# Kernel optimization log

Measured on AMD Instinct MI355X. Metric: run time of the kernel, lower is better.

## Reference

```python
import jax, jax.numpy as jnp
import numpy as np

NU, EU = 40000, 640000          # user-graph nodes / edges
B, T, NW, ET = 64, 16, 30, 60    # users, tweets/user, words/tweet, edges/tweet
NT = B * T * NW                  # 30720 tweet word-nodes
NTE = B * T * ET                 # 61440 tweet edges
NSEG_T = B * T                   # 1024 tweet segments


def gcn_conv(x, src, dst, W, b, N):
    """PyG GCNConv: x@W, add self loops, sym deg-normalize, scatter-add, +b."""
    x = x @ W
    loop = jnp.arange(N)
    s = jnp.concatenate([src, loop])
    d = jnp.concatenate([dst, loop])
    deg = jax.ops.segment_sum(jnp.ones_like(d, dtype=x.dtype), d, num_segments=N)
    dinv = jnp.where(deg > 0, jax.lax.rsqrt(deg), 0.0)
    norm = dinv[s] * dinv[d]                     # [E+N]
    out = jax.ops.segment_sum(x[s] * norm[:, None], d, num_segments=N)
    return out + b


def att_pool(x, seg, nseg, W1, b1, W2, b2):
    """AttentionalAggregation: gate_nn = Linear->Linear, segment softmax, weighted sum."""
    gate = (x @ W1 + b1) @ W2 + b2               # [N, C]
    m = jax.ops.segment_max(gate, seg, num_segments=nseg)
    e = jnp.exp(gate - m[seg])
    s = jax.ops.segment_sum(e, seg, num_segments=nseg)
    a = e / (s[seg] + 1e-16)
    return jax.ops.segment_sum(a * x, seg, num_segments=nseg)  # [nseg, C]


def gru_last(x_seq, W_ih, W_hh, b_ih, b_hh):
    """torch.nn.GRU, 1 layer; x_seq [B,T,C] -> final hidden [B,C]."""
    C = W_hh.shape[1]
    h0 = jnp.zeros((x_seq.shape[0], C), x_seq.dtype)
    def step(h, x):
        gi = x @ W_ih.T + b_ih
        gh = h @ W_hh.T + b_hh
        ir, iz, inn = jnp.split(gi, 3, axis=-1)
        hr, hz, hn = jnp.split(gh, 3, axis=-1)
        r = jax.nn.sigmoid(ir + hr)
        z = jax.nn.sigmoid(iz + hz)
        n = jnp.tanh(inn + r * hn)
        return (1.0 - z) * n + z * h, None
    hT, _ = jax.lax.scan(step, h0, jnp.swapaxes(x_seq, 0, 1))
    return hT


def setup_inputs():
    ks = jax.random.split(jax.random.key(0), 24)
    def rn(i, shape, s=1.0):
        return jax.random.normal(ks[i], shape, dtype=jnp.float32) * s
    z = lambda n_: jnp.zeros((n_,), jnp.float32)
    inp = {}
    inp["user_x"] = rn(0, (NU, 128))
    inp["user_feats"] = rn(1, (B, 32))
    inp["tweet_x"] = rn(2, (NT, 768))
    inp["Wu0"] = rn(3, (128, 128), 0.1); inp["bu0"] = z(128)
    inp["Wu1"] = rn(4, (128, 128), 0.1); inp["bu1"] = z(128)
    inp["Wgu1"] = rn(5, (128, 128), 0.1); inp["bgu1"] = z(128)
    inp["Wgu2"] = rn(6, (128, 128), 0.1); inp["bgu2"] = z(128)
    inp["Wt0"] = rn(7, (768, 256), 0.05); inp["bt0"] = z(256)
    inp["Wt1"] = rn(8, (256, 128), 0.1); inp["bt1"] = z(128)
    inp["Wgt1"] = rn(9, (128, 128), 0.1); inp["bgt1"] = z(128)
    inp["Wgt2"] = rn(10, (128, 128), 0.1); inp["bgt2"] = z(128)
    inp["W_ih"] = rn(11, (384, 128), 0.1); inp["b_ih"] = z(384)
    inp["W_hh"] = rn(12, (384, 128), 0.1); inp["b_hh"] = z(384)
    inp["Wd0"] = rn(13, (288, 256), 0.1); inp["bd0"] = z(256)
    inp["Wd1"] = rn(14, (256, 64), 0.1); inp["bd1"] = z(64)
    inp["Wp"] = rn(15, (64, 1), 0.1); inp["bp"] = z(1)
    inp["user_edge_index"] = jax.random.randint(ks[16], (2, EU), 0, NU)
    local = jax.random.randint(ks[17], (2, NTE), 0, NW)
    offs = jnp.repeat(jnp.arange(NSEG_T) * NW, ET)   # edges stay inside each tweet
    inp["tweet_edge_index"] = local + offs[None, :]
    inp["user_batch"] = jnp.arange(NU) // (NU // B)  # contiguous per-user segments (ptr)
    inp["tweet_batch"] = jnp.arange(NT) // NW        # contiguous per-tweet segments (ptr)
    return inp


def reference(user_x, user_feats, tweet_x,
              Wu0, bu0, Wu1, bu1, Wgu1, bgu1, Wgu2, bgu2,
              Wt0, bt0, Wt1, bt1, Wgt1, bgt1, Wgt2, bgt2,
              W_ih, b_ih, W_hh, b_hh,
              Wd0, bd0, Wd1, bd1, Wp, bp,
              user_edge_index, tweet_edge_index, user_batch, tweet_batch):
    h = jax.nn.relu(gcn_conv(user_x, user_edge_index[0], user_edge_index[1], Wu0, bu0, NU))
    h = jax.nn.relu(gcn_conv(h, user_edge_index[0], user_edge_index[1], Wu1, bu1, NU))
    user_pool = att_pool(h, user_batch, B, Wgu1, bgu1, Wgu2, bgu2)        # [B,128]
    g = jax.nn.relu(gcn_conv(tweet_x, tweet_edge_index[0], tweet_edge_index[1], Wt0, bt0, NT))
    g = jax.nn.relu(gcn_conv(g, tweet_edge_index[0], tweet_edge_index[1], Wt1, bt1, NT))
    tweet_pool = att_pool(g, tweet_batch, NSEG_T, Wgt1, bgt1, Wgt2, bgt2)  # [B*T,128]
    tweet_seq = tweet_pool.reshape(B, T, 128)
    tweet_h = gru_last(tweet_seq, W_ih, W_hh, b_ih, b_hh)                 # [B,128]
    # head
    full = jnp.concatenate([user_feats, user_pool, tweet_h], axis=1)      # [B,288]
    full = jax.nn.relu(full @ Wd0 + bd0)
    full = jax.nn.relu(full @ Wd1 + bd1)
    return jax.nn.sigmoid(full @ Wp + bp)                                 # [B,1]
```

## Files before the change

### kernel.cpp

```cpp
#include <hip/hip_runtime.h>
#include <hip/hip_bf16.h>

#define NU 40000
#define EU 640000
#define BB 64
#define TT 16
#define NW 30
#define NTNODES 30720
#define NTE 61440
#define NSEG_T 1024
#define NCHUNK 16

typedef __attribute__((ext_vector_type(8))) short bf16x8;
typedef __attribute__((ext_vector_type(4))) float f32x4;

__device__ __forceinline__ unsigned short f2bf(float x) {
    union { float f; unsigned u; } v; v.f = x;
    unsigned r = v.u + 0x7FFFu + ((v.u >> 16) & 1u);
    return (unsigned short)(r >> 16);
}
__device__ __forceinline__ float bf2f(unsigned short u) {
    union { unsigned u; float f; } v; v.u = (unsigned)u << 16; return v.f;
}
__device__ __forceinline__ void gld16(const unsigned short* g, unsigned short* l) {
    __builtin_amdgcn_global_load_lds(
        (const __attribute__((address_space(1))) void*)g,
        (__attribute__((address_space(3))) void*)l, 16, 0, 0);
}

__global__ void k_zeroint(int* __restrict__ p, int n) {
    int i = blockIdx.x * blockDim.x + threadIdx.x;
    if (i < n) p[i] = 0;
}

__global__ void k_hist2(const int* __restrict__ ue_dst, const int* __restrict__ te_dst,
                        int* __restrict__ hist_u, int* __restrict__ hist_t) {
    int i = blockIdx.x * blockDim.x + threadIdx.x;
    if (i < EU) atomicAdd(&hist_u[ue_dst[i]], 1);
    else if (i < EU + NTE) atomicAdd(&hist_t[te_dst[i - EU]], 1);
}

__global__ void k_dinv(const int* __restrict__ hist, float* __restrict__ dinv, int n) {
    int i = blockIdx.x * blockDim.x + threadIdx.x;
    if (i < n) dinv[i] = rsqrtf((float)hist[i] + 1.0f);
}

__global__ __launch_bounds__(256) void k_scan_a(const int* __restrict__ hist,
                                                int* __restrict__ bsum, int n) {
    __shared__ int red[256];
    int t = threadIdx.x;
    int i = blockIdx.x * 256 + t;
    red[t] = (i < n) ? hist[i] : 0;
    __syncthreads();
    for (int off = 128; off; off >>= 1) {
        if (t < off) red[t] += red[t + off];
        __syncthreads();
    }
    if (t == 0) bsum[blockIdx.x] = red[0];
}

__global__ __launch_bounds__(256) void k_scan_b(int* __restrict__ bsum, int nb) {
    __shared__ int s[256];
    int t = threadIdx.x;
    s[t] = (t < nb) ? bsum[t] : 0;
    __syncthreads();
    for (int off = 1; off < 256; off <<= 1) {
        int v = (t >= off) ? s[t - off] : 0;
        __syncthreads();
        s[t] += v;
        __syncthreads();
    }
    if (t < nb) bsum[t] = (t == 0) ? 0 : s[t - 1];
}

__global__ __launch_bounds__(256) void k_scan_c(const int* __restrict__ hist,
                                                const int* __restrict__ bsum,
                                                int* __restrict__ ptr,
                                                int* __restrict__ fill, int n) {
    __shared__ int s[256];
    int t = threadIdx.x;
    int i = blockIdx.x * 256 + t;
    int h = (i < n) ? hist[i] : 0;
    s[t] = h;
    __syncthreads();
    for (int off = 1; off < 256; off <<= 1) {
        int v = (t >= off) ? s[t - off] : 0;
        __syncthreads();
        s[t] += v;
        __syncthreads();
    }
    if (i < n) {
        int excl = bsum[blockIdx.x] + s[t] - h;
        ptr[i] = excl;
        fill[i] = excl;
        if (i == n - 1) ptr[n] = excl + h;
    }
}

__global__ void k_place(const int* __restrict__ src, const int* __restrict__ dst,
                        int* __restrict__ fill, int* __restrict__ esrc, int E) {
    int e = blockIdx.x * blockDim.x + threadIdx.x;
    if (e >= E) return;
    int d = dst[e];
    int pos = atomicAdd(&fill[d], 1);
    esrc[pos] = src[e];
}

__global__ void k_transpose(const float* __restrict__ in, float* __restrict__ out,
                            int R, int K) {
    int idx = blockIdx.x * blockDim.x + threadIdx.x;
    if (idx >= R * K) return;
    int j = idx / K, k = idx - j * K;
    out[k * R + j] = in[idx];
}

__device__ __forceinline__ void pack_one(const float* __restrict__ W,
                                         unsigned short* __restrict__ out,
                                         int f, int K, int N, int trans) {
    int j = f & 7;
    int chunk = f >> 3;
    int c = chunk & 511;
    int panel = chunk >> 9;
    int KS = K >> 5;
    int ks = panel % KS;
    int bn = panel / KS;
    int n = bn * 128 + (c & 127);
    int k = ks * 32 + (c >> 7) * 8 + j;
    float v = trans ? W[(size_t)n * K + k] : W[(size_t)k * N + n];
    out[f] = f2bf(v);
}

__global__ void k_packall(const float* __restrict__ Wu0, const float* __restrict__ Wu1,
                          const float* __restrict__ Wgu1, const float* __restrict__ Wgu2,
                          const float* __restrict__ Wt0, const float* __restrict__ Wt1,
                          const float* __restrict__ Wgt1, const float* __restrict__ Wgt2,
                          const float* __restrict__ Wih,
                          unsigned short* __restrict__ pk) {
    int f = blockIdx.x * blockDim.x + threadIdx.x;
    if (f < 16384)        pack_one(Wu0,  pk + 0,      f,          128, 128, 0);
    else if (f < 32768)   pack_one(Wu1,  pk + 16384,  f - 16384,  128, 128, 0);
    else if (f < 49152)   pack_one(Wgu1, pk + 32768,  f - 32768,  128, 128, 0);
    else if (f < 65536)   pack_one(Wgu2, pk + 49152,  f - 49152,  128, 128, 0);
    else if (f < 262144)  pack_one(Wt0,  pk + 65536,  f - 65536,  768, 256, 0);
    else if (f < 294912)  pack_one(Wt1,  pk + 262144, f - 262144, 256, 128, 0);
    else if (f < 311296)  pack_one(Wgt1, pk + 294912, f - 294912, 128, 128, 0);
    else if (f < 327680)  pack_one(Wgt2, pk + 311296, f - 311296, 128, 128, 0);
    else if (f < 376832)  pack_one(Wih,  pk + 327680, f - 327680, 128, 384, 1);
}

template<bool AF32>
__global__ __launch_bounds__(256) void k_mgemm(const void* __restrict__ Araw,
                                               const unsigned short* __restrict__ Bpk,
                                               const float* __restrict__ bias,
                                               void* __restrict__ Craw,
                                               int M, int K, int N, int flags) {
    constexpr int AST = AF32 ? 520 : 512;
    __shared__ unsigned short Alds[8 * AST];
    __shared__ unsigned short Blds[8192];
    int tid = threadIdx.x, lane = tid & 63, w = tid >> 6;
    int bm = blockIdx.x, bn = blockIdx.y;
    int wr = (w >> 1) * 32, wc = (w & 1) * 64;
    int l15 = lane & 15, lk = lane >> 4;

    f32x4 acc[2][4];
#pragma unroll
    for (int m = 0; m < 2; ++m)
#pragma unroll
        for (int n = 0; n < 4; ++n) acc[m][n] = (f32x4){0.f, 0.f, 0.f, 0.f};

    const unsigned short* Bpanel = Bpk + (size_t)bn * (K >> 5) * 4096;
    int KS64 = K >> 6;

    for (int ks = 0; ks < KS64; ++ks) {
        int k0 = ks * 64;
        {
            const unsigned short* bg = Bpanel + (size_t)ks * 8192;
#pragma unroll
            for (int q = 0; q < 4; ++q) {
                int off = (w * 4 + q) * 512;
                gld16(bg + off + lane * 8, &Blds[off]);
            }
        }
        if (AF32) {
            const float* A = (const float*)Araw;
#pragma unroll
            for (int p = 0; p < 4; ++p) {
                int f4 = p * 256 + tid;
                int row = f4 >> 4;
                int kq  = f4 & 15;
                float4 av = *(const float4*)(A + (size_t)(bm * 64 + row) * K + k0 + kq * 4);
                unsigned lo = (unsigned)f2bf(av.x) | ((unsigned)f2bf(av.y) << 16);
                unsigned hi = (unsigned)f2bf(av.z) | ((unsigned)f2bf(av.w) << 16);
                int off = (kq >> 1) * AST + row * 8 + (kq & 1) * 4;
                *(uint2*)&Alds[off] = make_uint2(lo, hi);
            }
        } else {
            const unsigned short* A = (const unsigned short*)Araw;
#pragma unroll
            for (int q = 0; q < 2; ++q) {
                int kblk = w * 2 + q;
                gld16(A + (size_t)(bm * 64 + lane) * K + k0 + kblk * 8,
                      &Alds[kblk * 512]);
            }
        }
        __syncthreads();
#pragma unroll
        for (int h = 0; h < 2; ++h) {
            int kb = h * 4 + lk;
            bf16x8 a[2], b[4];
#pragma unroll
            for (int m = 0; m < 2; ++m)
                a[m] = *(const bf16x8*)&Alds[kb * AST + (wr + m * 16 + l15) * 8];
#pragma unroll
            for (int n = 0; n < 4; ++n)
                b[n] = *(const bf16x8*)&Blds[kb * 1024 + (wc + n * 16 + l15) * 8];
#pragma unroll
            for (int m = 0; m < 2; ++m)
#pragma unroll
                for (int n = 0; n < 4; ++n)
                    acc[m][n] = __builtin_amdgcn_mfma_f32_16x16x32_bf16(a[m], b[n], acc[m][n], 0, 0, 0);
        }
        __syncthreads();
    }

#pragma unroll
    for (int m = 0; m < 2; ++m) {
        int grow0 = bm * 64 + wr + m * 16 + lk * 4;
#pragma unroll
        for (int n = 0; n < 4; ++n) {
            int gcol = bn * 128 + wc + n * 16 + l15;
            float bv = (flags & 1) ? bias[gcol] : 0.f;
#pragma unroll
            for (int i = 0; i < 4; ++i) {
                int grow = grow0 + i;
                float v = acc[m][n][i] + bv;
                if (flags & 2) v = fmaxf(v, 0.f);
                if (flags & 4) ((float*)Craw)[(size_t)grow * N + gcol] = v;
                else ((unsigned short*)Craw)[(size_t)grow * N + gcol] = f2bf(v);
            }
        }
    }
}

__global__ __launch_bounds__(256) void k_gagg(const unsigned short* __restrict__ y,
                                              const int* __restrict__ ptr,
                                              const int* __restrict__ esrc,
                                              const float* __restrict__ dinv,
                                              const float* __restrict__ bias,
                                              unsigned short* __restrict__ ob, int N, int nch) {
    int idx = blockIdx.x * 4 + (threadIdx.x >> 6);
    if (idx >= N * nch) return;
    int v = idx / nch, ch = idx - v * nch;
    int C = nch << 7;
    int lane = threadIdx.x & 63;
    int c0 = (ch << 7) + lane * 2;
    float dv = dinv[v];
    unsigned yv = *(const unsigned*)(y + (size_t)v * C + c0);
    float a0 = dv * dv * bf2f((unsigned short)yv);
    float a1 = dv * dv * bf2f((unsigned short)(yv >> 16));
    int e = ptr[v], e1 = ptr[v + 1];
    for (; e + 3 < e1; e += 4) {
        int s0 = esrc[e], s1 = esrc[e + 1], s2 = esrc[e + 2], s3 = esrc[e + 3];
        float cc0 = dv * dinv[s0], cc1 = dv * dinv[s1];
        float cc2 = dv * dinv[s2], cc3 = dv * dinv[s3];
        unsigned w0 = *(const unsigned*)(y + (size_t)s0 * C + c0);
        unsigned w1 = *(const unsigned*)(y + (size_t)s1 * C + c0);
        unsigned w2 = *(const unsigned*)(y + (size_t)s2 * C + c0);
        unsigned w3 = *(const unsigned*)(y + (size_t)s3 * C + c0);
        a0 += cc0 * bf2f((unsigned short)w0) + cc1 * bf2f((unsigned short)w1)
            + cc2 * bf2f((unsigned short)w2) + cc3 * bf2f((unsigned short)w3);
        a1 += cc0 * bf2f((unsigned short)(w0 >> 16)) + cc1 * bf2f((unsigned short)(w1 >> 16))
            + cc2 * bf2f((unsigned short)(w2 >> 16)) + cc3 * bf2f((unsigned short)(w3 >> 16));
    }
    for (; e < e1; ++e) {
        int s0 = esrc[e];
        float cc0 = dv * dinv[s0];
        unsigned w0 = *(const unsigned*)(y + (size_t)s0 * C + c0);
        a0 += cc0 * bf2f((unsigned short)w0);
        a1 += cc0 * bf2f((unsigned short)(w0 >> 16));
    }
    a0 = fmaxf(a0 + bias[c0], 0.f);
    a1 = fmaxf(a1 + bias[c0 + 1], 0.f);
    *(unsigned*)(ob + (size_t)v * C + c0) = (unsigned)f2bf(a0) | ((unsigned)f2bf(a1) << 16);
}

__global__ __launch_bounds__(128) void k_attpool(const unsigned short* __restrict__ x,
                                                 const unsigned short* __restrict__ gate,
                                                 unsigned short* __restrict__ outb, int S) {
    int seg = blockIdx.x;
    int c = threadIdx.x;
    size_t base = (size_t)seg * S * 128 + c;
    float m = -1e30f;
    for (int n = 0; n < S; ++n) m = fmaxf(m, bf2f(gate[base + (size_t)n * 128]));
    float se = 0.f, acc = 0.f;
    for (int n = 0; n < S; ++n) {
        float g = bf2f(gate[base + (size_t)n * 128]);
        float e = expf(g - m);
        se += e;
        acc += e * bf2f(x[base + (size_t)n * 128]);
    }
    outb[(size_t)seg * 128 + c] = f2bf(acc / (se + 1e-16f));
}

__global__ __launch_bounds__(256) void k_pool_pmax(const unsigned short* __restrict__ gate,
                                                   float* __restrict__ pmax, int S) {
    int seg = blockIdx.x, ch = blockIdx.y;
    int c = threadIdx.x & 127, j = threadIdx.x >> 7;
    int csz = (S + NCHUNK - 1) / NCHUNK;
    int n0 = ch * csz, n1 = min(S, n0 + csz);
    size_t base = (size_t)seg * S * 128 + c;
    float m = -1e30f;
    for (int n = n0 + j; n < n1; n += 2)
        m = fmaxf(m, bf2f(gate[base + (size_t)n * 128]));
    __shared__ float red[2][128];
    red[j][c] = m;
    __syncthreads();
    if (j == 0)
        pmax[((size_t)seg * NCHUNK + ch) * 128 + c] = fmaxf(red[0][c], red[1][c]);
}

__global__ __launch_bounds__(128) void k_pool_cmax(const float* __restrict__ pmax,
                                                   float* __restrict__ gmax) {
    int seg = blockIdx.x, c = threadIdx.x;
    float m = -1e30f;
    for (int ch = 0; ch < NCHUNK; ++ch)
        m = fmaxf(m, pmax[((size_t)seg * NCHUNK + ch) * 128 + c]);
    gmax[(size_t)seg * 128 + c] = m;
}

__global__ __launch_bounds__(256) void k_pool_psum(const unsigned short* __restrict__ x,
                                                   const unsigned short* __restrict__ gate,
                                                   const float* __restrict__ gmax,
                                                   float* __restrict__ pse,
                                                   float* __restrict__ pacc, int S) {
    int seg = blockIdx.x, ch = blockIdx.y;
    int c = threadIdx.x & 127, j = threadIdx.x >> 7;
    int csz = (S + NCHUNK - 1) / NCHUNK;
    int n0 = ch * csz, n1 = min(S, n0 + csz);
    size_t base = (size_t)seg * S * 128 + c;
    float m = gmax[(size_t)seg * 128 + c];
    float se = 0.f, acc = 0.f;
    for (int n = n0 + j; n < n1; n += 2) {
        float g = bf2f(gate[base + (size_t)n * 128]);
        float e = expf(g - m);
        se += e;
        acc += e * bf2f(x[base + (size_t)n * 128]);
    }
    __shared__ float rs[2][128], ra[2][128];
    rs[j][c] = se; ra[j][c] = acc;
    __syncthreads();
    if (j == 0) {
        size_t o = ((size_t)seg * NCHUNK + ch) * 128 + c;
        pse[o]  = rs[0][c] + rs[1][c];
        pacc[o] = ra[0][c] + ra[1][c];
    }
}

__global__ __launch_bounds__(128) void k_pool_final(const float* __restrict__ pse,
                                                    const float* __restrict__ pacc,
                                                    float* __restrict__ out) {
    int seg = blockIdx.x, c = threadIdx.x;
    float se = 0.f, acc = 0.f;
    for (int ch = 0; ch < NCHUNK; ++ch) {
        size_t o = ((size_t)seg * NCHUNK + ch) * 128 + c;
        se += pse[o];
        acc += pacc[o];
    }
    out[(size_t)seg * 128 + c] = acc / (se + 1e-16f);
}

__global__ __launch_bounds__(768) void k_gru_rec(const float* __restrict__ gi,
                                                 const float* __restrict__ whhT,
                                                 const float* __restrict__ bhh,
                                                 float* __restrict__ hT) {
    __shared__ float hs[128];
    __shared__ float ph[768];
    int b = blockIdx.x, t = threadIdx.x;
    int half = (t >= 384) ? 1 : 0;
    int j = t - half * 384;
    float w[64];
#pragma unroll
    for (int i = 0; i < 64; ++i)
        w[i] = whhT[(half * 64 + i) * 384 + j];
    float chr = 0.f, chz = 0.f, chn = 0.f;
    if (t < 128) {
        hs[t] = 0.f;
        chr = bhh[t]; chz = bhh[128 + t]; chn = bhh[256 + t];
    }
    __syncthreads();
    for (int step = 0; step < TT; ++step) {
        float a0 = 0.f, a1 = 0.f, a2 = 0.f, a3 = 0.f;
        const float* hbase = hs + half * 64;
#pragma unroll
        for (int i = 0; i < 64; i += 4) {
            float4 hv = *(const float4*)(hbase + i);
            a0 += hv.x * w[i + 0];
            a1 += hv.y * w[i + 1];
            a2 += hv.z * w[i + 2];
            a3 += hv.w * w[i + 3];
        }
        ph[t] = (a0 + a1) + (a2 + a3);
        __syncthreads();
        float hnew = 0.f;
        if (t < 128) {
            const float* girow = gi + ((size_t)b * TT + step) * 384;
            float hr = ph[t] + ph[t + 384] + chr;
            float hz = ph[128 + t] + ph[512 + t] + chz;
            float hn = ph[256 + t] + ph[640 + t] + chn;
            float ir = girow[t], iz = girow[128 + t], in = girow[256 + t];
            float r = 1.f / (1.f + expf(-(ir + hr)));
            float z = 1.f / (1.f + expf(-(iz + hz)));
            float n = tanhf(in + r * hn);
            hnew = (1.f - z) * n + z * hs[t];
        }
        __syncthreads();
        if (t < 128) hs[t] = hnew;
        __syncthreads();
    }
    if (t < 128) hT[(size_t)b * 128 + t] = hs[t];
}

__global__ __launch_bounds__(256) void k_head(const float* __restrict__ uf,
                                              const float* __restrict__ up,
                                              const float* __restrict__ th,
                                              const float* __restrict__ Wd0, const float* __restrict__ bd0,
                                              const float* __restrict__ Wd1, const float* __restrict__ bd1,
                                              const float* __restrict__ Wp, const float* __restrict__ bp,
                                              float* __restrict__ out) {
    __shared__ float in0[288], l1[256], l2[64];
    int b = blockIdx.x, t = threadIdx.x;
    if (t < 32) in0[t] = uf[b * 32 + t];
    else if (t < 160) in0[t] = up[b * 128 + (t - 32)];
    if (t < 128) in0[160 + t] = th[b * 128 + t];
    __syncthreads();
    float acc = bd0[t];
    for (int k = 0; k < 288; ++k) acc += in0[k] * Wd0[k * 256 + t];
    l1[t] = fmaxf(acc, 0.f);
    __syncthreads();
    if (t < 64) {
        float a2 = bd1[t];
        for (int k = 0; k < 256; ++k) a2 += l1[k] * Wd1[k * 64 + t];
        l2[t] = fmaxf(a2, 0.f);
    }
    __syncthreads();
    if (t < 64) {
        float p = l2[t] * Wp[t];
        for (int off = 32; off; off >>= 1) p += __shfl_down(p, off, 64);
        if (t == 0) out[b] = 1.f / (1.f + expf(-(p + bp[0])));
    }
}

extern "C" void kernel_launch(void* const* d_in, const int* in_sizes, int n_in,
                              void* d_out, int out_size, void* d_ws, size_t ws_size,
                              hipStream_t stream) {
    const float* user_x     = (const float*)d_in[0];
    const float* user_feats = (const float*)d_in[1];
    const float* tweet_x    = (const float*)d_in[2];
    const float* Wu0 = (const float*)d_in[3];  const float* bu0 = (const float*)d_in[4];
    const float* Wu1 = (const float*)d_in[5];  const float* bu1 = (const float*)d_in[6];
    const float* Wgu1 = (const float*)d_in[7]; const float* bgu1 = (const float*)d_in[8];
    const float* Wgu2 = (const float*)d_in[9]; const float* bgu2 = (const float*)d_in[10];
    const float* Wt0 = (const float*)d_in[11]; const float* bt0 = (const float*)d_in[12];
    const float* Wt1 = (const float*)d_in[13]; const float* bt1 = (const float*)d_in[14];
    const float* Wgt1 = (const float*)d_in[15]; const float* bgt1 = (const float*)d_in[16];
    const float* Wgt2 = (const float*)d_in[17]; const float* bgt2 = (const float*)d_in[18];
    const float* W_ih = (const float*)d_in[19]; const float* b_ih = (const float*)d_in[20];
    const float* W_hh = (const float*)d_in[21]; const float* b_hh = (const float*)d_in[22];
    const float* Wd0 = (const float*)d_in[23]; const float* bd0 = (const float*)d_in[24];
    const float* Wd1 = (const float*)d_in[25]; const float* bd1 = (const float*)d_in[26];
    const float* Wp  = (const float*)d_in[27]; const float* bp  = (const float*)d_in[28];
    const int* ue = (const int*)d_in[29];
    const int* te = (const int*)d_in[30];
    const int* ue_src = ue, *ue_dst = ue + EU;
    const int* te_src = te, *te_dst = te + NTE;

    float* ws = (float*)d_ws;
    size_t o = 0;
    float* dinv_u = ws + o;     o += NU;
    float* dinv_t = ws + o;     o += NTNODES;
    float* user_pool = ws + o;  o += (size_t)BB * 128;
    float* tweet_h = ws + o;    o += (size_t)BB * 128;
    float* whhT = ws + o;       o += 128 * 384;
    float* gi = ws + o;         o += (size_t)NSEG_T * 384;
    float* pmax = ws + o;       o += 131072;
    float* pse = ws + o;        o += 131072;
    float* pacc = ws + o;       o += 131072;
    float* gmax = ws + o;       o += 8192;
    int* iw = (int*)(ws + o);
    int* hist_u = iw;
    int* hist_t = iw + NU;
    int* ptr_u  = iw + NU + NTNODES;
    int* fill_u = ptr_u + NU + 1;
    int* esrc_u = fill_u + NU;
    int* ptr_t  = esrc_u + EU;
    int* fill_t = ptr_t + NTNODES + 1;
    int* esrc_t = fill_t + NTNODES;
    int* bsum_u = esrc_t + NTE;
    int* bsum_t = bsum_u + 256;
    unsigned short* pk = (unsigned short*)(((uintptr_t)(bsum_t + 256) + 15) & ~(uintptr_t)15);
    unsigned short* pWu0  = pk;
    unsigned short* pWu1  = pWu0  + 16384;
    unsigned short* pWgu1 = pWu1  + 16384;
    unsigned short* pWgu2 = pWgu1 + 16384;
    unsigned short* pWt0  = pWgu2 + 16384;
    unsigned short* pWt1  = pWt0  + 196608;
    unsigned short* pWgt1 = pWt1  + 32768;
    unsigned short* pWgt2 = pWgt1 + 16384;
    unsigned short* pWih  = pWgt2 + 16384;
    unsigned short* arena = (unsigned short*)(((uintptr_t)(pWih + 49152) + 15) & ~(uintptr_t)15);
    const size_t SLOT = (size_t)NTNODES * 256;
    unsigned short* P0 = arena;
    unsigned short* P1 = P0 + SLOT;
    unsigned short* P2 = P1 + SLOT;
    unsigned short* P3 = P2 + SLOT;
    unsigned short* tpool_bf = P3 + SLOT;
    float* out = (float*)d_out;

    dim3 b256(256);
    const int NBU = (NU + 255) / 256;
    const int NBT = (NTNODES + 255) / 256;
    const int GMU = NU / 64;
    const int GMT = NTNODES / 64;
    const float* NB = nullptr;

    hipLaunchKernelGGL(k_packall, dim3((376832 + 255) / 256), b256, 0, stream,
                       Wu0, Wu1, Wgu1, Wgu2, Wt0, Wt1, Wgt1, Wgt2, W_ih, pk);
    hipLaunchKernelGGL(k_transpose, dim3((384 * 128 + 255) / 256), b256, 0, stream,
                       W_hh, whhT, 384, 128);

    hipLaunchKernelGGL(k_zeroint, dim3((NU + NTNODES + 255) / 256), b256, 0, stream,
                       hist_u, NU + NTNODES);
    hipLaunchKernelGGL(k_hist2, dim3((EU + NTE + 255) / 256), b256, 0, stream,
                       ue_dst, te_dst, hist_u, hist_t);
    hipLaunchKernelGGL(k_dinv, dim3((NU + NTNODES + 255) / 256), b256, 0, stream,
                       hist_u, dinv_u, NU + NTNODES);
    hipLaunchKernelGGL(k_scan_a, dim3(NBU), b256, 0, stream, hist_u, bsum_u, NU);
    hipLaunchKernelGGL(k_scan_b, dim3(1), b256, 0, stream, bsum_u, NBU);
    hipLaunchKernelGGL(k_scan_c, dim3(NBU), b256, 0, stream, hist_u, bsum_u, ptr_u, fill_u, NU);
    hipLaunchKernelGGL(k_place, dim3((EU + 255) / 256), b256, 0, stream,
                       ue_src, ue_dst, fill_u, esrc_u, EU);
    hipLaunchKernelGGL(k_scan_a, dim3(NBT), b256, 0, stream, hist_t, bsum_t, NTNODES);
    hipLaunchKernelGGL(k_scan_b, dim3(1), b256, 0, stream, bsum_t, NBT);
    hipLaunchKernelGGL(k_scan_c, dim3(NBT), b256, 0, stream, hist_t, bsum_t, ptr_t, fill_t, NTNODES);
    hipLaunchKernelGGL(k_place, dim3((NTE + 255) / 256), b256, 0, stream,
                       te_src, te_dst, fill_t, esrc_t, NTE);

    hipLaunchKernelGGL(HIP_KERNEL_NAME(k_mgemm<true>), dim3(GMT, 2), b256, 0, stream,
                       (const void*)tweet_x, pWt0, NB, (void*)P0, NTNODES, 768, 256, 0);
    hipLaunchKernelGGL(k_gagg, dim3((NTNODES * 2 + 3) / 4), b256, 0, stream,
                       P0, ptr_t, esrc_t, dinv_t, bt0, P1, NTNODES, 2);

    hipLaunchKernelGGL(HIP_KERNEL_NAME(k_mgemm<true>), dim3(GMU, 1), b256, 0, stream,
                       (const void*)user_x, pWu0, NB, (void*)P3, NU, 128, 128, 0);
    hipLaunchKernelGGL(k_gagg, dim3((NU + 3) / 4), b256, 0, stream,
                       P3, ptr_u, esrc_u, dinv_u, bu0, P0, NU, 1);
    hipLaunchKernelGGL(HIP_KERNEL_NAME(k_mgemm<false>), dim3(GMU, 1), b256, 0, stream,
                       (const void*)P0, pWu1, NB, (void*)P2, NU, 128, 128, 0);
    hipLaunchKernelGGL(k_gagg, dim3((NU + 3) / 4), b256, 0, stream,
                       P2, ptr_u, esrc_u, dinv_u, bu1, P3, NU, 1);
    hipLaunchKernelGGL(HIP_KERNEL_NAME(k_mgemm<false>), dim3(GMU, 1), b256, 0, stream,
                       (const void*)P3, pWgu1, bgu1, (void*)P2, NU, 128, 128, 1);
    hipLaunchKernelGGL(HIP_KERNEL_NAME(k_mgemm<false>), dim3(GMU, 1), b256, 0, stream,
                       (const void*)P2, pWgu2, bgu2, (void*)P0, NU, 128, 128, 1);
    hipLaunchKernelGGL(k_pool_pmax, dim3(BB, NCHUNK), b256, 0, stream, P0, pmax, NU / BB);
    hipLaunchKernelGGL(k_pool_cmax, dim3(BB), dim3(128), 0, stream, pmax, gmax);
    hipLaunchKernelGGL(k_pool_psum, dim3(BB, NCHUNK), b256, 0, stream,
                       P3, P0, gmax, pse, pacc, NU / BB);
    hipLaunchKernelGGL(k_pool_final, dim3(BB), dim3(128), 0, stream, pse, pacc, user_pool);

    const size_t T128 = (size_t)NTNODES * 128;
    hipLaunchKernelGGL(HIP_KERNEL_NAME(k_mgemm<false>), dim3(GMT, 1), b256, 0, stream,
                       (const void*)P1, pWt1, NB, (void*)P2, NTNODES, 256, 128, 0);
    hipLaunchKernelGGL(k_gagg, dim3((NTNODES + 3) / 4), b256, 0, stream,
                       P2, ptr_t, esrc_t, dinv_t, bt1, P3, NTNODES, 1);
    hipLaunchKernelGGL(HIP_KERNEL_NAME(k_mgemm<false>), dim3(GMT, 1), b256, 0, stream,
                       (const void*)P3, pWgt1, bgt1, (void*)P1, NTNODES, 128, 128, 1);
    hipLaunchKernelGGL(HIP_KERNEL_NAME(k_mgemm<false>), dim3(GMT, 1), b256, 0, stream,
                       (const void*)P1, pWgt2, bgt2, (void*)(P1 + T128), NTNODES, 128, 128, 1);
    hipLaunchKernelGGL(k_attpool, dim3(NSEG_T), dim3(128), 0, stream,
                       P3, P1 + T128, tpool_bf, NW);

    hipLaunchKernelGGL(HIP_KERNEL_NAME(k_mgemm<false>), dim3(NSEG_T / 64, 3), b256, 0, stream,
                       (const void*)tpool_bf, pWih, b_ih, (void*)gi, NSEG_T, 128, 384, 5);
    hipLaunchKernelGGL(k_gru_rec, dim3(BB), dim3(768), 0, stream,
                       gi, whhT, b_hh, tweet_h);

    hipLaunchKernelGGL(k_head, dim3(BB), b256, 0, stream,
                       user_feats, user_pool, tweet_h,
                       Wd0, bd0, Wd1, bd1, Wp, bp, out);
}
```

Baseline: 372.4 us.

## Fuse graph preprocessing kernels, fuse gate GEMM pairs, shrink GEMM M tile

Merges the user and tweet CSR-building kernels (scan, place) into combined launches and folds the degree rsqrt into the scan. Adds a fused two-layer gate kernel that keeps the intermediate activation in LDS rather than writing it to global memory. Removes the separate max-combine kernel by recomputing the max inside psum. Halves the generic GEMM tile height to 32 rows to launch more blocks, which lowers per-block MFMA reuse. Together these cut launch count and intermediate traffic.

```diff
diff --git a/kernel.cpp b/kernel.cpp
--- a/kernel.cpp
+++ b/kernel.cpp
@@ -10,6 +10,8 @@
 #define NTE 61440
 #define NSEG_T 1024
 #define NCHUNK 16
+#define NBU 157
+#define NBT 120
 
 typedef __attribute__((ext_vector_type(8))) short bf16x8;
 typedef __attribute__((ext_vector_type(4))) float f32x4;
@@ -40,29 +42,31 @@
     else if (i < EU + NTE) atomicAdd(&hist_t[te_dst[i - EU]], 1);
 }
 
-__global__ void k_dinv(const int* __restrict__ hist, float* __restrict__ dinv, int n) {
-    int i = blockIdx.x * blockDim.x + threadIdx.x;
-    if (i < n) dinv[i] = rsqrtf((float)hist[i] + 1.0f);
-}
-
-__global__ __launch_bounds__(256) void k_scan_a(const int* __restrict__ hist,
-                                                int* __restrict__ bsum, int n) {
+__global__ __launch_bounds__(256) void k_scan_a2(const int* __restrict__ hist_u,
+                                                 int* __restrict__ bsum_u,
+                                                 int* __restrict__ bsum_t) {
     __shared__ int red[256];
-    int t = threadIdx.x;
-    int i = blockIdx.x * 256 + t;
-    red[t] = (i < n) ? hist[i] : 0;
+    int b = blockIdx.x, t = threadIdx.x;
+    const int* h; int* bs; int n, lb;
+    if (b < NBU) { h = hist_u;      bs = bsum_u; n = NU;      lb = b; }
+    else         { h = hist_u + NU; bs = bsum_t; n = NTNODES; lb = b - NBU; }
+    int i = lb * 256 + t;
+    red[t] = (i < n) ? h[i] : 0;
     __syncthreads();
     for (int off = 128; off; off >>= 1) {
         if (t < off) red[t] += red[t + off];
         __syncthreads();
     }
-    if (t == 0) bsum[blockIdx.x] = red[0];
-}
-
-__global__ __launch_bounds__(256) void k_scan_b(int* __restrict__ bsum, int nb) {
+    if (t == 0) bs[lb] = red[0];
+}
+
+__global__ __launch_bounds__(256) void k_scan_b2(int* __restrict__ bsum_u,
+                                                 int* __restrict__ bsum_t) {
     __shared__ int s[256];
     int t = threadIdx.x;
-    s[t] = (t < nb) ? bsum[t] : 0;
+    int* bs = blockIdx.x ? bsum_t : bsum_u;
+    int nb  = blockIdx.x ? NBT : NBU;
+    s[t] = (t < nb) ? bs[t] : 0;
     __syncthreads();
     for (int off = 1; off < 256; off <<= 1) {
         int v = (t >= off) ? s[t - off] : 0;
@@ -70,18 +74,23 @@
         s[t] += v;
         __syncthreads();
     }
-    if (t < nb) bsum[t] = (t == 0) ? 0 : s[t - 1];
-}
-
-__global__ __launch_bounds__(256) void k_scan_c(const int* __restrict__ hist,
-                                                const int* __restrict__ bsum,
-                                                int* __restrict__ ptr,
-                                                int* __restrict__ fill, int n) {
+    if (t < nb) bs[t] = (t == 0) ? 0 : s[t - 1];
+}
+
+__global__ __launch_bounds__(256) void k_scan_c2(const int* __restrict__ hist_u,
+                                                 const int* __restrict__ bsum_u,
+                                                 const int* __restrict__ bsum_t,
+                                                 int* __restrict__ ptr_u, int* __restrict__ fill_u,
+                                                 int* __restrict__ ptr_t, int* __restrict__ fill_t,
+                                                 float* __restrict__ dinv_u) {
     __shared__ int s[256];
-    int t = threadIdx.x;
-    int i = blockIdx.x * 256 + t;
-    int h = (i < n) ? hist[i] : 0;
-    s[t] = h;
+    int b = blockIdx.x, t = threadIdx.x;
+    const int *h, *bs; int *ptr, *fill; int n, lb; float* dv;
+    if (b < NBU) { h = hist_u;      bs = bsum_u; ptr = ptr_u; fill = fill_u; n = NU;      lb = b;       dv = dinv_u; }
+    else         { h = hist_u + NU; bs = bsum_t; ptr = ptr_t; fill = fill_t; n = NTNODES; lb = b - NBU; dv = dinv_u + NU; }
+    int i = lb * 256 + t;
+    int hv = (i < n) ? h[i] : 0;
+    s[t] = hv;
     __syncthreads();
     for (int off = 1; off < 256; off <<= 1) {
         int v = (t >= off) ? s[t - off] : 0;
@@ -90,20 +99,27 @@
         __syncthreads();
     }
     if (i < n) {
-        int excl = bsum[blockIdx.x] + s[t] - h;
+        int excl = bs[lb] + s[t] - hv;
         ptr[i] = excl;
         fill[i] = excl;
-        if (i == n - 1) ptr[n] = excl + h;
-    }
-}
-
-__global__ void k_place(const int* __restrict__ src, const int* __restrict__ dst,
-                        int* __restrict__ fill, int* __restrict__ esrc, int E) {
+        dv[i] = rsqrtf((float)hv + 1.0f);
+        if (i == n - 1) ptr[n] = excl + hv;
+    }
+}
+
+__global__ void k_place2(const int* __restrict__ ue_src, const int* __restrict__ ue_dst,
+                         const int* __restrict__ te_src, const int* __restrict__ te_dst,
+                         int* __restrict__ fill_u, int* __restrict__ esrc_u,
+                         int* __restrict__ fill_t, int* __restrict__ esrc_t) {
     int e = blockIdx.x * blockDim.x + threadIdx.x;
-    if (e >= E) return;
-    int d = dst[e];
-    int pos = atomicAdd(&fill[d], 1);
-    esrc[pos] = src[e];
+    if (e < EU) {
+        int pos = atomicAdd(&fill_u[ue_dst[e]], 1);
+        esrc_u[pos] = ue_src[e];
+    } else if (e < EU + NTE) {
+        int e2 = e - EU;
+        int pos = atomicAdd(&fill_t[te_dst[e2]], 1);
+        esrc_t[pos] = te_src[e2];
+    }
 }
 
 __global__ void k_transpose(const float* __restrict__ in, float* __restrict__ out,
@@ -154,19 +170,17 @@
                                                const float* __restrict__ bias,
                                                void* __restrict__ Craw,
                                                int M, int K, int N, int flags) {
-    constexpr int AST = AF32 ? 520 : 512;
+    constexpr int AST = AF32 ? 260 : 256;
     __shared__ unsigned short Alds[8 * AST];
     __shared__ unsigned short Blds[8192];
     int tid = threadIdx.x, lane = tid & 63, w = tid >> 6;
     int bm = blockIdx.x, bn = blockIdx.y;
-    int wr = (w >> 1) * 32, wc = (w & 1) * 64;
+    int wr = (w >> 1) * 16, wc = (w & 1) * 64;
     int l15 = lane & 15, lk = lane >> 4;
 
-    f32x4 acc[2][4];
-#pragma unroll
-    for (int m = 0; m < 2; ++m)
-#pragma unroll
-        for (int n = 0; n < 4; ++n) acc[m][n] = (f32x4){0.f, 0.f, 0.f, 0.f};
+    f32x4 acc[4];
+#pragma unroll
+    for (int n = 0; n < 4; ++n) acc[n] = (f32x4){0.f, 0.f, 0.f, 0.f};
 
     const unsigned short* Bpanel = Bpk + (size_t)bn * (K >> 5) * 4096;
     int KS64 = K >> 6;
@@ -184,11 +198,11 @@
         if (AF32) {
             const float* A = (const float*)Araw;
 #pragma unroll
-            for (int p = 0; p < 4; ++p) {
+            for (int p = 0; p < 2; ++p) {
                 int f4 = p * 256 + tid;
                 int row = f4 >> 4;
                 int kq  = f4 & 15;
-                float4 av = *(const float4*)(A + (size_t)(bm * 64 + row) * K + k0 + kq * 4);
+                float4 av = *(const float4*)(A + (size_t)(bm * 32 + row) * K + k0 + kq * 4);
                 unsigned lo = (unsigned)f2bf(av.x) | ((unsigned)f2bf(av.y) << 16);
                 unsigned hi = (unsigned)f2bf(av.z) | ((unsigned)f2bf(av.w) << 16);
                 int off = (kq >> 1) * AST + row * 8 + (kq & 1) * 4;
@@ -196,12 +210,74 @@
             }
         } else {
             const unsigned short* A = (const unsigned short*)Araw;
-#pragma unroll
-            for (int q = 0; q < 2; ++q) {
-                int kblk = w * 2 + q;
-                gld16(A + (size_t)(bm * 64 + lane) * K + k0 + kblk * 8,
-                      &Alds[kblk * 512]);
-            }
+            int kblk = 2 * w + (lane >> 5);
+            int row = lane & 31;
+            gld16(A + (size_t)(bm * 32 + row) * K + k0 + kblk * 8,
+                  &Alds[w * 512]);
+        }
+        __syncthreads();
+#pragma unroll
+        for (int h = 0; h < 2; ++h) {
+            int kb = h * 4 + lk;
+            bf16x8 a = *(const bf16x8*)&Alds[kb * AST + (wr + l15) * 8];
+            bf16x8 b[4];
+#pragma unroll
+            for (int n = 0; n < 4; ++n)
+                b[n] = *(const bf16x8*)&Blds[kb * 1024 + (wc + n * 16 + l15) * 8];
+#pragma unroll
+            for (int n = 0; n < 4; ++n)
+                acc[n] = __builtin_amdgcn_mfma_f32_16x16x32_bf16(a, b[n], acc[n], 0, 0, 0);
+        }
+        __syncthreads();
+    }
+
+    int grow0 = bm * 32 + wr + lk * 4;
+#pragma unroll
+    for (int n = 0; n < 4; ++n) {
+        int gcol = bn * 128 + wc + n * 16 + l15;
+        float bv = (flags & 1) ? bias[gcol] : 0.f;
+#pragma unroll
+        for (int i = 0; i < 4; ++i) {
+            int grow = grow0 + i;
+            float v = acc[n][i] + bv;
+            if (flags & 2) v = fmaxf(v, 0.f);
+            if (flags & 4) ((float*)Craw)[(size_t)grow * N + gcol] = v;
+            else ((unsigned short*)Craw)[(size_t)grow * N + gcol] = f2bf(v);
+        }
+    }
+}
+
+__global__ __launch_bounds__(256) void k_gatepair(const unsigned short* __restrict__ X,
+                                                  const unsigned short* __restrict__ W1,
+                                                  const float* __restrict__ b1,
+                                                  const unsigned short* __restrict__ W2,
+                                                  const float* __restrict__ b2,
+                                                  unsigned short* __restrict__ outp, int M) {
+    __shared__ unsigned short Ax[16 * 512];
+    __shared__ unsigned short Wl[8192];
+    int tid = threadIdx.x, lane = tid & 63, w = tid >> 6;
+    int bm = blockIdx.x;
+    int wr = (w >> 1) * 32, wc = (w & 1) * 64;
+    int l15 = lane & 15, lk = lane >> 4;
+
+#pragma unroll
+    for (int q = 0; q < 4; ++q) {
+        int pl = w * 4 + q;
+        gld16(X + (size_t)(bm * 64 + lane) * 128 + pl * 8, &Ax[pl * 512]);
+    }
+
+    f32x4 acc[2][4];
+#pragma unroll
+    for (int m = 0; m < 2; ++m)
+#pragma unroll
+        for (int n = 0; n < 4; ++n) acc[m][n] = (f32x4){0.f, 0.f, 0.f, 0.f};
+
+    for (int ks = 0; ks < 2; ++ks) {
+        const unsigned short* wp = W1 + ks * 8192;
+#pragma unroll
+        for (int q = 0; q < 4; ++q) {
+            int off = (w * 4 + q) * 512;
+            gld16(wp + off + lane * 8, &Wl[off]);
         }
         __syncthreads();
 #pragma unroll
@@ -210,10 +286,10 @@
             bf16x8 a[2], b[4];
 #pragma unroll
             for (int m = 0; m < 2; ++m)
-                a[m] = *(const bf16x8*)&Alds[kb * AST + (wr + m * 16 + l15) * 8];
+                a[m] = *(const bf16x8*)&Ax[(ks * 8 + kb) * 512 + (wr + m * 16 + l15) * 8];
 #pragma unroll
             for (int n = 0; n < 4; ++n)
-                b[n] = *(const bf16x8*)&Blds[kb * 1024 + (wc + n * 16 + l15) * 8];
+                b[n] = *(const bf16x8*)&Wl[kb * 1024 + (wc + n * 16 + l15) * 8];
 #pragma unroll
             for (int m = 0; m < 2; ++m)
 #pragma unroll
@@ -224,22 +300,64 @@
     }
 
 #pragma unroll
-    for (int m = 0; m < 2; ++m) {
-        int grow0 = bm * 64 + wr + m * 16 + lk * 4;
+    for (int m = 0; m < 2; ++m)
 #pragma unroll
         for (int n = 0; n < 4; ++n) {
-            int gcol = bn * 128 + wc + n * 16 + l15;
-            float bv = (flags & 1) ? bias[gcol] : 0.f;
+            int col = wc + n * 16 + l15;
+            float bv = b1[col];
 #pragma unroll
             for (int i = 0; i < 4; ++i) {
-                int grow = grow0 + i;
+                int row = wr + m * 16 + lk * 4 + i;
                 float v = acc[m][n][i] + bv;
-                if (flags & 2) v = fmaxf(v, 0.f);
-                if (flags & 4) ((float*)Craw)[(size_t)grow * N + gcol] = v;
-                else ((unsigned short*)Craw)[(size_t)grow * N + gcol] = f2bf(v);
+                Ax[(col >> 3) * 512 + row * 8 + (col & 7)] = f2bf(v);
             }
         }
-    }
+    __syncthreads();
+
+#pragma unroll
+    for (int m = 0; m < 2; ++m)
+#pragma unroll
+        for (int n = 0; n < 4; ++n) acc[m][n] = (f32x4){0.f, 0.f, 0.f, 0.f};
+    for (int ks = 0; ks < 2; ++ks) {
+        const unsigned short* wp = W2 + ks * 8192;
+#pragma unroll
+        for (int q = 0; q < 4; ++q) {
+            int off = (w * 4 + q) * 512;
+            gld16(wp + off + lane * 8, &Wl[off]);
+        }
+        __syncthreads();
+#pragma unroll
+        for (int h = 0; h < 2; ++h) {
+            int kb = h * 4 + lk;
+            bf16x8 a[2], b[4];
+#pragma unroll
+            for (int m = 0; m < 2; ++m)
+                a[m] = *(const bf16x8*)&Ax[(ks * 8 + kb) * 512 + (wr + m * 16 + l15) * 8];
+#pragma unroll
+            for (int n = 0; n < 4; ++n)
+                b[n] = *(const bf16x8*)&Wl[kb * 1024 + (wc + n * 16 + l15) * 8];
+#pragma unroll
+            for (int m = 0; m < 2; ++m)
+#pragma unroll
+                for (int n = 0; n < 4; ++n)
+                    acc[m][n] = __builtin_amdgcn_mfma_f32_16x16x32_bf16(a[m], b[n], acc[m][n], 0, 0, 0);
+        }
+        __syncthreads();
+    }
+
+#pragma unroll
+    for (int m = 0; m < 2; ++m)
+#pragma unroll
+        for (int n = 0; n < 4; ++n) {
+            int col = wc + n * 16 + l15;
+            float bv = b2[col];
+#pragma unroll
+            for (int i = 0; i < 4; ++i) {
+                int row = bm * 64 + wr + m * 16 + lk * 4 + i;
+                float v = acc[m][n][i] + bv;
+                outp[(size_t)row * 128 + col] = f2bf(v);
+            }
+        }
 }
 
 __global__ __launch_bounds__(256) void k_gagg(const unsigned short* __restrict__ y,
@@ -319,18 +437,9 @@
         pmax[((size_t)seg * NCHUNK + ch) * 128 + c] = fmaxf(red[0][c], red[1][c]);
 }
 
-__global__ __launch_bounds__(128) void k_pool_cmax(const float* __restrict__ pmax,
-                                                   float* __restrict__ gmax) {
-    int seg = blockIdx.x, c = threadIdx.x;
-    float m = -1e30f;
-    for (int ch = 0; ch < NCHUNK; ++ch)
-        m = fmaxf(m, pmax[((size_t)seg * NCHUNK + ch) * 128 + c]);
-    gmax[(size_t)seg * 128 + c] = m;
-}
-
 __global__ __launch_bounds__(256) void k_pool_psum(const unsigned short* __restrict__ x,
                                                    const unsigned short* __restrict__ gate,
-                                                   const float* __restrict__ gmax,
+                                                   const float* __restrict__ pmax,
                                                    float* __restrict__ pse,
                                                    float* __restrict__ pacc, int S) {
     int seg = blockIdx.x, ch = blockIdx.y;
@@ -338,7 +447,10 @@
     int csz = (S + NCHUNK - 1) / NCHUNK;
     int n0 = ch * csz, n1 = min(S, n0 + csz);
     size_t base = (size_t)seg * S * 128 + c;
-    float m = gmax[(size_t)seg * 128 + c];
+    float m = -1e30f;
+#pragma unroll
+    for (int ch2 = 0; ch2 < NCHUNK; ++ch2)
+        m = fmaxf(m, pmax[((size_t)seg * NCHUNK + ch2) * 128 + c]);
     float se = 0.f, acc = 0.f;
     for (int n = n0 + j; n < n1; n += 2) {
         float g = bf2f(gate[base + (size_t)n * 128]);
@@ -485,7 +597,6 @@
     float* pmax = ws + o;       o += 131072;
     float* pse = ws + o;        o += 131072;
     float* pacc = ws + o;       o += 131072;
-    float* gmax = ws + o;       o += 8192;
     int* iw = (int*)(ws + o);
     int* hist_u = iw;
     int* hist_t = iw + NU;
@@ -517,10 +628,8 @@
     float* out = (float*)d_out;
 
     dim3 b256(256);
-    const int NBU = (NU + 255) / 256;
-    const int NBT = (NTNODES + 255) / 256;
-    const int GMU = NU / 64;
-    const int GMT = NTNODES / 64;
+    const int GMU = NU / 32;
+    const int GMT = NTNODES / 32;
     const float* NB = nullptr;
 
     hipLaunchKernelGGL(k_packall, dim3((376832 + 255) / 256), b256, 0, stream,
@@ -532,18 +641,12 @@
                        hist_u, NU + NTNODES);
     hipLaunchKernelGGL(k_hist2, dim3((EU + NTE + 255) / 256), b256, 0, stream,
                        ue_dst, te_dst, hist_u, hist_t);
-    hipLaunchKernelGGL(k_dinv, dim3((NU + NTNODES + 255) / 256), b256, 0, stream,
-                       hist_u, dinv_u, NU + NTNODES);
-    hipLaunchKernelGGL(k_scan_a, dim3(NBU), b256, 0, stream, hist_u, bsum_u, NU);
-    hipLaunchKernelGGL(k_scan_b, dim3(1), b256, 0, stream, bsum_u, NBU);
-    hipLaunchKernelGGL(k_scan_c, dim3(NBU), b256, 0, stream, hist_u, bsum_u, ptr_u, fill_u, NU);
-    hipLaunchKernelGGL(k_place, dim3((EU + 255) / 256), b256, 0, stream,
-                       ue_src, ue_dst, fill_u, esrc_u, EU);
-    hipLaunchKernelGGL(k_scan_a, dim3(NBT), b256, 0, stream, hist_t, bsum_t, NTNODES);
-    hipLaunchKernelGGL(k_scan_b, dim3(1), b256, 0, stream, bsum_t, NBT);
-    hipLaunchKernelGGL(k_scan_c, dim3(NBT), b256, 0, stream, hist_t, bsum_t, ptr_t, fill_t, NTNODES);
-    hipLaunchKernelGGL(k_place, dim3((NTE + 255) / 256), b256, 0, stream,
-                       te_src, te_dst, fill_t, esrc_t, NTE);
+    hipLaunchKernelGGL(k_scan_a2, dim3(NBU + NBT), b256, 0, stream, hist_u, bsum_u, bsum_t);
+    hipLaunchKernelGGL(k_scan_b2, dim3(2), b256, 0, stream, bsum_u, bsum_t);
+    hipLaunchKernelGGL(k_scan_c2, dim3(NBU + NBT), b256, 0, stream,
+                       hist_u, bsum_u, bsum_t, ptr_u, fill_u, ptr_t, fill_t, dinv_u);
+    hipLaunchKernelGGL(k_place2, dim3((EU + NTE + 255) / 256), b256, 0, stream,
+                       ue_src, ue_dst, te_src, te_dst, fill_u, esrc_u, fill_t, esrc_t);
 
     hipLaunchKernelGGL(HIP_KERNEL_NAME(k_mgemm<true>), dim3(GMT, 2), b256, 0, stream,
                        (const void*)tweet_x, pWt0, NB, (void*)P0, NTNODES, 768, 256, 0);
@@ -558,29 +661,23 @@
                        (const void*)P0, pWu1, NB, (void*)P2, NU, 128, 128, 0);
     hipLaunchKernelGGL(k_gagg, dim3((NU + 3) / 4), b256, 0, stream,
                        P2, ptr_u, esrc_u, dinv_u, bu1, P3, NU, 1);
-    hipLaunchKernelGGL(HIP_KERNEL_NAME(k_mgemm<false>), dim3(GMU, 1), b256, 0, stream,
-                       (const void*)P3, pWgu1, bgu1, (void*)P2, NU, 128, 128, 1);
-    hipLaunchKernelGGL(HIP_KERNEL_NAME(k_mgemm<false>), dim3(GMU, 1), b256, 0, stream,
-                       (const void*)P2, pWgu2, bgu2, (void*)P0, NU, 128, 128, 1);
+    hipLaunchKernelGGL(k_gatepair, dim3(NU / 64), b256, 0, stream,
+                       P3, pWgu1, bgu1, pWgu2, bgu2, P0, NU);
     hipLaunchKernelGGL(k_pool_pmax, dim3(BB, NCHUNK), b256, 0, stream, P0, pmax, NU / BB);
-    hipLaunchKernelGGL(k_pool_cmax, dim3(BB), dim3(128), 0, stream, pmax, gmax);
     hipLaunchKernelGGL(k_pool_psum, dim3(BB, NCHUNK), b256, 0, stream,
-                       P3, P0, gmax, pse, pacc, NU / BB);
+                       P3, P0, pmax, pse, pacc, NU / BB);
     hipLaunchKernelGGL(k_pool_final, dim3(BB), dim3(128), 0, stream, pse, pacc, user_pool);
 
-    const size_t T128 = (size_t)NTNODES * 128;
     hipLaunchKernelGGL(HIP_KERNEL_NAME(k_mgemm<false>), dim3(GMT, 1), b256, 0, stream,
                        (const void*)P1, pWt1, NB, (void*)P2, NTNODES, 256, 128, 0);
     hipLaunchKernelGGL(k_gagg, dim3((NTNODES + 3) / 4), b256, 0, stream,
                        P2, ptr_t, esrc_t, dinv_t, bt1, P3, NTNODES, 1);
-    hipLaunchKernelGGL(HIP_KERNEL_NAME(k_mgemm<false>), dim3(GMT, 1), b256, 0, stream,
-                       (const void*)P3, pWgt1, bgt1, (void*)P1, NTNODES, 128, 128, 1);
-    hipLaunchKernelGGL(HIP_KERNEL_NAME(k_mgemm<false>), dim3(GMT, 1), b256, 0, stream,
-                       (const void*)P1, pWgt2, bgt2, (void*)(P1 + T128), NTNODES, 128, 128, 1);
+    hipLaunchKernelGGL(k_gatepair, dim3(NTNODES / 64), b256, 0, stream,
+                       P3, pWgt1, bgt1, pWgt2, bgt2, P1, NTNODES);
     hipLaunchKernelGGL(k_attpool, dim3(NSEG_T), dim3(128), 0, stream,
-                       P3, P1 + T128, tpool_bf, NW);
-
-    hipLaunchKernelGGL(HIP_KERNEL_NAME(k_mgemm<false>), dim3(NSEG_T / 64, 3), b256, 0, stream,
+                       P3, P1, tpool_bf, NW);
+
+    hipLaunchKernelGGL(HIP_KERNEL_NAME(k_mgemm<false>), dim3(NSEG_T / 32, 3), b256, 0, stream,
                        (const void*)tpool_bf, pWih, b_ih, (void*)gi, NSEG_T, 128, 384, 5);
     hipLaunchKernelGGL(k_gru_rec, dim3(BB), dim3(768), 0, stream,
                        gi, whhT, b_hh, tweet_h);
```

New measurement: 345.1 us. 1.08x faster.
